# Kernel optimization log

Measured on AMD Instinct MI355X. Metric: run time of the kernel, lower is better.

Reference implementation:

```python
import jax, jax.numpy as jnp
import numpy as np

B, S, D, H = 4, 1024, 1024, 16
DH = D // H  # 64, per-head dim; FFN hidden = 2048
DFF = 2048

def setup_inputs() -> dict:
    key = jax.random.key(0)
    ks = jax.random.split(key, 6)
    x = jax.random.normal(ks[0], (B, S, D), dtype=jnp.float32)
    # Per-head q/k/v projection weights, stacked over heads: [H, D, DH].
    # Equivalent math to n_heads separate SelfAttentionLayer(d_head) calls + concat.
    sc_in = 1.0 / np.sqrt(D)
    Wq = jax.random.normal(ks[1], (H, D, DH), dtype=jnp.float32) * sc_in
    Wk = jax.random.normal(ks[2], (H, D, DH), dtype=jnp.float32) * sc_in
    Wv = jax.random.normal(ks[3], (H, D, DH), dtype=jnp.float32) * sc_in
    W1 = jax.random.normal(ks[4], (D, DFF), dtype=jnp.float32) * sc_in
    b1 = jnp.zeros((DFF,), dtype=jnp.float32)
    W2 = jax.random.normal(ks[5], (DFF, D), dtype=jnp.float32) * (1.0 / np.sqrt(DFF))
    b2 = jnp.zeros((D,), dtype=jnp.float32)
    return {"x": x, "Wq": Wq, "Wk": Wk, "Wv": Wv,
            "W1": W1, "b1": b1, "W2": W2, "b2": b2}

def reference(x, Wq, Wk, Wv, W1, b1, W2, b2):
    # Batched multi-head self-attention (math-equivalent to the per-head loop + concat).
    q = jnp.einsum('bsd,hde->bhse', x, Wq)          # [B,H,S,DH]
    k = jnp.einsum('bsd,hde->bhse', x, Wk)
    v = jnp.einsum('bsd,hde->bhse', x, Wv)
    scale = 1.0 / jnp.sqrt(jnp.asarray(q.shape[-1], q.dtype))
    scores = jnp.einsum('bhqe,bhke->bhqk', q, k) * scale  # [B,H,S,S]
    attn = jax.nn.softmax(scores, axis=-1)
    o = jnp.einsum('bhqk,bhke->bhqe', attn, v)      # [B,H,S,DH]
    h1 = o.transpose(0, 2, 1, 3).reshape(x.shape[0], x.shape[1], -1)  # concat heads -> [B,S,D]
    # FCLayer(2048, d): Dense(2048, relu) -> Dense(d)
    y = jax.nn.relu(h1 @ W1 + b1) @ W2 + b2
    return y
```

## Files before the change

kernel.cpp:

```cpp
#include <hip/hip_runtime.h>
#include <hip/hip_bf16.h>


typedef unsigned short u16;
typedef __attribute__((ext_vector_type(8))) short bfrag8;
typedef __attribute__((ext_vector_type(4))) float f32x4;

constexpr int Bb = 4, Ss = 1024, Dd = 1024, Hh = 16, DFF = 2048;

__device__ __forceinline__ u16 f2bf(float f) {
  unsigned u = __float_as_uint(f);
  return (u16)((u + 0x7fffu + ((u >> 16) & 1u)) >> 16);
}

__device__ __forceinline__ int swz(int byte) {
  return byte ^ (((byte >> 7) & 7) << 4);
}

__device__ __forceinline__ void gload16(const void* g, void* l) {
  __builtin_amdgcn_global_load_lds(
      (const __attribute__((address_space(1))) unsigned int*)g,
      (__attribute__((address_space(3))) unsigned int*)l, 16, 0, 0);
}

__global__ __launch_bounds__(256) void cvt_bf16(const float* __restrict__ in,
                                                u16* __restrict__ out, int n4) {
  int i = blockIdx.x * 256 + threadIdx.x;
  if (i >= n4) return;
  float4 v = ((const float4*)in)[i];
  ushort4 o = make_ushort4(f2bf(v.x), f2bf(v.y), f2bf(v.z), f2bf(v.w));
  *(ushort4*)(out + (size_t)i * 4) = o;
}

__device__ __forceinline__ void transpose64(const float* __restrict__ in,
                                            u16* __restrict__ out,
                                            int R, int C, int r0, int c0) {
  __shared__ float tile[64][65];
  const int t = threadIdx.x, cl = t & 63, rq = t >> 6;
#pragma unroll
  for (int i = 0; i < 16; ++i) {
    int rl = rq * 16 + i;
    tile[rl][cl] = in[(size_t)(r0 + rl) * C + c0 + cl];
  }
  __syncthreads();
#pragma unroll
  for (int i = 0; i < 16; ++i) {
    int oc = rq * 16 + i;
    out[(size_t)(c0 + oc) * R + r0 + cl] = f2bf(tile[cl][oc]);
  }
}

__global__ __launch_bounds__(256) void transpose_cvt(const float* __restrict__ in,
                                                     u16* __restrict__ out,
                                                     int R, int C) {
  transpose64(in, out, R, C, blockIdx.x * 64, blockIdx.y * 64);
}

__global__ __launch_bounds__(256) void qkv_transpose_cvt(
    const float* __restrict__ Wq, const float* __restrict__ Wk,
    const float* __restrict__ Wv, u16* __restrict__ out) {
  const int z = blockIdx.y;
  const int which = z >> 4, h = z & 15;
  const float* in = (which == 0 ? Wq : which == 1 ? Wk : Wv) + (size_t)h * 1024 * 64;
  u16* o = out + (size_t)z * 64 * 1024;
  transpose64(in, o, 1024, 64, blockIdx.x * 64, 0);
}

template <int EPI>
__global__ __launch_bounds__(256) void mfma_gemm(
    const u16* __restrict__ A, const u16* __restrict__ Bt,
    const float* __restrict__ bias, void* __restrict__ Cout, int N, int K) {
  __shared__ alignas(16) u16 Asm[128 * 32];
  __shared__ alignas(16) u16 Bsm[128 * 32];
  const int tid = threadIdx.x;
  const int wid = tid >> 6, lane = tid & 63;
  const int m0 = blockIdx.y * 128, n0 = blockIdx.x * 128;
  const int wr = wid >> 1, wc = wid & 1;
  const int fr = lane & 15, krow = lane >> 4;

  const int srow = tid >> 2;
  const int sk = (tid & 3) * 8;
  const u16* ga0 = A + (size_t)(m0 + srow) * K + sk;
  const u16* ga1 = A + (size_t)(m0 + srow + 64) * K + sk;
  const u16* gb0 = Bt + (size_t)(n0 + srow) * K + sk;
  const u16* gb1 = Bt + (size_t)(n0 + srow + 64) * K + sk;
  char* lA0 = (char*)Asm + tid * 16;
  char* lA1 = lA0 + 4096;
  char* lB0 = (char*)Bsm + tid * 16;
  char* lB1 = lB0 + 4096;

  f32x4 acc[4][4];
#pragma unroll
  for (int i = 0; i < 4; ++i)
#pragma unroll
    for (int j = 0; j < 4; ++j) acc[i][j] = (f32x4){0.f, 0.f, 0.f, 0.f};

  const char* pa = (const char*)Asm + (wr * 64 + fr) * 64 + krow * 16;
  const char* pb = (const char*)Bsm + (wc * 64 + fr) * 64 + krow * 16;

  for (int kt = 0; kt < K / 32; ++kt) {
    __syncthreads();
    gload16(ga0 + kt * 32, lA0);
    gload16(ga1 + kt * 32, lA1);
    gload16(gb0 + kt * 32, lB0);
    gload16(gb1 + kt * 32, lB1);
    __syncthreads();

    bfrag8 af[4], bfv[4];
#pragma unroll
    for (int i = 0; i < 4; ++i) af[i] = *(const bfrag8*)(pa + i * 1024);
#pragma unroll
    for (int j = 0; j < 4; ++j) bfv[j] = *(const bfrag8*)(pb + j * 1024);
#pragma unroll
    for (int i = 0; i < 4; ++i)
#pragma unroll
      for (int j = 0; j < 4; ++j)
        acc[i][j] = __builtin_amdgcn_mfma_f32_16x16x32_bf16(af[i], bfv[j], acc[i][j], 0, 0, 0);
  }

  const int orow = (lane >> 4) * 4;
  const int ocol = lane & 15;
#pragma unroll
  for (int i = 0; i < 4; ++i) {
#pragma unroll
    for (int j = 0; j < 4; ++j) {
      const int gn = n0 + wc * 64 + j * 16 + ocol;
      const int gm0 = m0 + wr * 64 + i * 16 + orow;
      if (EPI == 0) {
        const int which = gn >> 10, hh = (gn >> 6) & 15, e = gn & 63;
        const int bb = gm0 >> 10, s0 = gm0 & 1023;
        const int hb = hh * 4 + bb;
        u16* oq = (u16*)Cout;
        if (which < 2) {
#pragma unroll
          for (int r = 0; r < 4; ++r)
            oq[(size_t)which * 4194304 + ((size_t)hb * 1024 + s0 + r) * 64 + e] =
                f2bf(acc[i][j][r]);
        } else {
          ushort4 pk = make_ushort4(f2bf(acc[i][j][0]), f2bf(acc[i][j][1]),
                                    f2bf(acc[i][j][2]), f2bf(acc[i][j][3]));
          *(ushort4*)&oq[8388608 + ((size_t)hb * 64 + e) * 1024 + s0] = pk;
        }
      } else if (EPI == 1) {
#pragma unroll
        for (int r = 0; r < 4; ++r) {
          float v = fmaxf(acc[i][j][r] + bias[gn], 0.f);
          ((u16*)Cout)[(size_t)(gm0 + r) * N + gn] = f2bf(v);
        }
      } else {
#pragma unroll
        for (int r = 0; r < 4; ++r)
          ((float*)Cout)[(size_t)(gm0 + r) * N + gn] = acc[i][j][r] + bias[gn];
      }
    }
  }
}

__global__ __launch_bounds__(256) void attn_mfma(
    const u16* __restrict__ qb, const u16* __restrict__ kb,
    const u16* __restrict__ vtb, u16* __restrict__ h1) {
  __shared__ alignas(16) u16 Ks[64 * 64];
  __shared__ alignas(16) u16 Vs[64 * 64];
  __shared__ alignas(16) u16 Ps[4][32 * 64];
  const int tid = threadIdx.x, wid = tid >> 6, lane = tid & 63;
  const int hb = blockIdx.y, h = hb >> 2, b = hb & 3;
  const int q0 = blockIdx.x * 128 + wid * 32;
  const int fr = lane & 15, hi = lane >> 4;

  const u16* Qg = qb + ((size_t)hb * 1024 + q0) * 64;
  const u16* Kg = kb + (size_t)hb * 1024 * 64;
  const u16* Vg = vtb + (size_t)hb * 64 * 1024;
  char* Kw = (char*)Ks;
  char* Vw = (char*)Vs;
  char* Pw = (char*)Ps[wid];

  bfrag8 qf[2][2];
#pragma unroll
  for (int m = 0; m < 2; ++m)
#pragma unroll
    for (int kk = 0; kk < 2; ++kk)
      qf[m][kk] = *(const bfrag8*)(Qg + (m * 16 + fr) * 64 + kk * 32 + hi * 8);

  f32x4 acc_o[2][4];
#pragma unroll
  for (int m = 0; m < 2; ++m)
#pragma unroll
    for (int en = 0; en < 4; ++en) acc_o[m][en] = (f32x4){0.f, 0.f, 0.f, 0.f};
  float mrun[2][4], lrun[2][4];
#pragma unroll
  for (int m = 0; m < 2; ++m)
#pragma unroll
    for (int r = 0; r < 4; ++r) { mrun[m][r] = -3.0e38f; lrun[m][r] = 0.f; }

  const int srow0 = tid >> 3;
  const int scol = (tid & 7) * 8;

  for (int kt = 0; kt < 16; ++kt) {
    __syncthreads();
    bfrag8 kv0 = *(const bfrag8*)(Kg + (size_t)(kt * 64 + srow0) * 64 + scol);
    bfrag8 kv1 = *(const bfrag8*)(Kg + (size_t)(kt * 64 + srow0 + 32) * 64 + scol);
    bfrag8 vv0 = *(const bfrag8*)(Vg + (size_t)srow0 * 1024 + kt * 64 + scol);
    bfrag8 vv1 = *(const bfrag8*)(Vg + (size_t)(srow0 + 32) * 1024 + kt * 64 + scol);
    *(bfrag8*)(Kw + swz(srow0 * 128 + scol * 2)) = kv0;
    *(bfrag8*)(Kw + swz((srow0 + 32) * 128 + scol * 2)) = kv1;
    *(bfrag8*)(Vw + swz(srow0 * 128 + scol * 2)) = vv0;
    *(bfrag8*)(Vw + swz((srow0 + 32) * 128 + scol * 2)) = vv1;
    __syncthreads();

    f32x4 sc[2][4];
#pragma unroll
    for (int m = 0; m < 2; ++m)
#pragma unroll
      for (int kn = 0; kn < 4; ++kn) sc[m][kn] = (f32x4){0.f, 0.f, 0.f, 0.f};
    bfrag8 kf[4][2];
#pragma unroll
    for (int kn = 0; kn < 4; ++kn)
#pragma unroll
      for (int kk = 0; kk < 2; ++kk)
        kf[kn][kk] = *(const bfrag8*)(Kw + swz((kn * 16 + fr) * 128 + kk * 64 + hi * 16));
#pragma unroll
    for (int m = 0; m < 2; ++m)
#pragma unroll
      for (int kn = 0; kn < 4; ++kn)
#pragma unroll
        for (int kk = 0; kk < 2; ++kk)
          sc[m][kn] = __builtin_amdgcn_mfma_f32_16x16x32_bf16(qf[m][kk], kf[kn][kk],
                                                              sc[m][kn], 0, 0, 0);

#pragma unroll
    for (int m = 0; m < 2; ++m) {
      float ss[4][4];
#pragma unroll
      for (int kn = 0; kn < 4; ++kn)
#pragma unroll
        for (int r = 0; r < 4; ++r) ss[kn][r] = sc[m][kn][r] * 0.125f;
      float rmax[4];
#pragma unroll
      for (int r = 0; r < 4; ++r)
        rmax[r] = fmaxf(fmaxf(ss[0][r], ss[1][r]), fmaxf(ss[2][r], ss[3][r]));
#pragma unroll
      for (int mk = 1; mk <= 8; mk <<= 1)
#pragma unroll
        for (int r = 0; r < 4; ++r)
          rmax[r] = fmaxf(rmax[r], __shfl_xor(rmax[r], mk));
      float scl[4];
#pragma unroll
      for (int r = 0; r < 4; ++r) {
        const float mnew = fmaxf(mrun[m][r], rmax[r]);
        scl[r] = __expf(mrun[m][r] - mnew);
        mrun[m][r] = mnew;
      }
#pragma unroll
      for (int kn = 0; kn < 4; ++kn)
#pragma unroll
        for (int r = 0; r < 4; ++r) ss[kn][r] = __expf(ss[kn][r] - mrun[m][r]);
      float ps[4];
#pragma unroll
      for (int r = 0; r < 4; ++r)
        ps[r] = (ss[0][r] + ss[1][r]) + (ss[2][r] + ss[3][r]);
#pragma unroll
      for (int mk = 1; mk <= 8; mk <<= 1)
#pragma unroll
        for (int r = 0; r < 4; ++r) ps[r] += __shfl_xor(ps[r], mk);
#pragma unroll
      for (int r = 0; r < 4; ++r) lrun[m][r] = lrun[m][r] * scl[r] + ps[r];
#pragma unroll
      for (int en = 0; en < 4; ++en)
#pragma unroll
        for (int r = 0; r < 4; ++r) acc_o[m][en][r] *= scl[r];
#pragma unroll
      for (int kn = 0; kn < 4; ++kn)
#pragma unroll
        for (int r = 0; r < 4; ++r)
          *(u16*)(Pw + swz((m * 16 + hi * 4 + r) * 128 + (kn * 16 + fr) * 2)) =
              f2bf(ss[kn][r]);
    }

    bfrag8 vf[4][2], pf[2][2];
#pragma unroll
    for (int en = 0; en < 4; ++en)
#pragma unroll
      for (int kf2 = 0; kf2 < 2; ++kf2)
        vf[en][kf2] = *(const bfrag8*)(Vw + swz((en * 16 + fr) * 128 + kf2 * 64 + hi * 16));
#pragma unroll
    for (int m = 0; m < 2; ++m)
#pragma unroll
      for (int kf2 = 0; kf2 < 2; ++kf2)
        pf[m][kf2] = *(const bfrag8*)(Pw + swz((m * 16 + fr) * 128 + kf2 * 64 + hi * 16));
#pragma unroll
    for (int m = 0; m < 2; ++m)
#pragma unroll
      for (int en = 0; en < 4; ++en)
#pragma unroll
        for (int kf2 = 0; kf2 < 2; ++kf2)
          acc_o[m][en] = __builtin_amdgcn_mfma_f32_16x16x32_bf16(pf[m][kf2], vf[en][kf2],
                                                                 acc_o[m][en], 0, 0, 0);
  }

#pragma unroll
  for (int m = 0; m < 2; ++m) {
    float inv[4];
#pragma unroll
    for (int r = 0; r < 4; ++r) inv[r] = 1.f / lrun[m][r];
#pragma unroll
    for (int en = 0; en < 4; ++en)
#pragma unroll
      for (int r = 0; r < 4; ++r) {
        const int s = q0 + m * 16 + hi * 4 + r;
        h1[((size_t)(b * 1024 + s)) * 1024 + h * 64 + en * 16 + fr] =
            f2bf(acc_o[m][en][r] * inv[r]);
      }
  }
}

extern "C" void kernel_launch(void* const* d_in, const int* in_sizes, int n_in,
                              void* d_out, int out_size, void* d_ws, size_t ws_size,
                              hipStream_t stream) {
  const float* x  = (const float*)d_in[0];
  const float* Wq = (const float*)d_in[1];
  const float* Wk = (const float*)d_in[2];
  const float* Wv = (const float*)d_in[3];
  const float* W1 = (const float*)d_in[4];
  const float* b1 = (const float*)d_in[5];
  const float* W2 = (const float*)d_in[6];
  const float* b2 = (const float*)d_in[7];

  const size_t MB = 1u << 20;
  char* w = (char*)d_ws;
  u16* qkvb  = (u16*)w;
  u16* Xb    = (u16*)(w + 24 * MB);
  u16* Wqkvt = (u16*)(w + 32 * MB);
  u16* W1t   = (u16*)(w + 38 * MB);
  u16* W2t   = (u16*)(w + 42 * MB);
  u16* h1b   = (u16*)(w + 46 * MB);
  u16* ffb   = (u16*)(w + 54 * MB);

  cvt_bf16<<<4096, 256, 0, stream>>>(x, Xb, 1048576);
  qkv_transpose_cvt<<<dim3(16, 48), 256, 0, stream>>>(Wq, Wk, Wv, Wqkvt);
  transpose_cvt<<<dim3(16, 32), 256, 0, stream>>>(W1, W1t, 1024, 2048);
  transpose_cvt<<<dim3(32, 16), 256, 0, stream>>>(W2, W2t, 2048, 1024);

  mfma_gemm<0><<<dim3(24, 32), 256, 0, stream>>>(Xb, Wqkvt, nullptr, qkvb, 3072, 1024);
  attn_mfma<<<dim3(8, 64), 256, 0, stream>>>(qkvb, qkvb + 4194304, qkvb + 8388608, h1b);
  mfma_gemm<1><<<dim3(16, 32), 256, 0, stream>>>(h1b, W1t, b1, ffb, 2048, 1024);
  mfma_gemm<2><<<dim3(8, 32), 256, 0, stream>>>(ffb, W2t, b2, d_out, 1024, 2048);
}
```

Measured before the change: 277.6 us.

## Rewrite attention to register-resident exp2 softmax, add XCD block swizzle and N64 GEMM

```diff
diff --git a/kernel.cpp b/kernel.cpp
--- a/kernel.cpp
+++ b/kernel.cpp
@@ -5,22 +5,26 @@
 typedef unsigned short u16;
 typedef __attribute__((ext_vector_type(8))) short bfrag8;
 typedef __attribute__((ext_vector_type(4))) float f32x4;
+typedef __attribute__((ext_vector_type(4))) int ix4;
 
 constexpr int Bb = 4, Ss = 1024, Dd = 1024, Hh = 16, DFF = 2048;
+constexpr float QSCALE = 0.18033688011112042f;
 
 __device__ __forceinline__ u16 f2bf(float f) {
   unsigned u = __float_as_uint(f);
   return (u16)((u + 0x7fffu + ((u >> 16) & 1u)) >> 16);
-}
-
-__device__ __forceinline__ int swz(int byte) {
-  return byte ^ (((byte >> 7) & 7) << 4);
 }
 
 __device__ __forceinline__ void gload16(const void* g, void* l) {
   __builtin_amdgcn_global_load_lds(
       (const __attribute__((address_space(1))) unsigned int*)g,
       (__attribute__((address_space(3))) unsigned int*)l, 16, 0, 0);
+}
+
+__device__ __forceinline__ int xcd_swz() {
+  const int id = blockIdx.y * gridDim.x + blockIdx.x;
+  const int cpx = (gridDim.x * gridDim.y) >> 3;
+  return (id & 7) * cpx + (id >> 3);
 }
 
 __global__ __launch_bounds__(256) void cvt_bf16(const float* __restrict__ in,
@@ -74,7 +78,8 @@
   __shared__ alignas(16) u16 Bsm[128 * 32];
   const int tid = threadIdx.x;
   const int wid = tid >> 6, lane = tid & 63;
-  const int m0 = blockIdx.y * 128, n0 = blockIdx.x * 128;
+  const int nid = xcd_swz();
+  const int m0 = (nid / gridDim.x) * 128, n0 = (nid % gridDim.x) * 128;
   const int wr = wid >> 1, wc = wid & 1;
   const int fr = lane & 15, krow = lane >> 4;
 
@@ -131,11 +136,14 @@
         const int bb = gm0 >> 10, s0 = gm0 & 1023;
         const int hb = hh * 4 + bb;
         u16* oq = (u16*)Cout;
-        if (which < 2) {
+        if (which == 0) {
 #pragma unroll
           for (int r = 0; r < 4; ++r)
-            oq[(size_t)which * 4194304 + ((size_t)hb * 1024 + s0 + r) * 64 + e] =
-                f2bf(acc[i][j][r]);
+            oq[((size_t)hb * 1024 + s0 + r) * 64 + e] = f2bf(acc[i][j][r] * QSCALE);
+        } else if (which == 1) {
+#pragma unroll
+          for (int r = 0; r < 4; ++r)
+            oq[4194304 + ((size_t)hb * 1024 + s0 + r) * 64 + e] = f2bf(acc[i][j][r]);
         } else {
           ushort4 pk = make_ushort4(f2bf(acc[i][j][0]), f2bf(acc[i][j][1]),
                                     f2bf(acc[i][j][2]), f2bf(acc[i][j][3]));
@@ -156,23 +164,81 @@
   }
 }
 
-__global__ __launch_bounds__(256) void attn_mfma(
+__global__ __launch_bounds__(256) void mfma_gemm_n64(
+    const u16* __restrict__ A, const u16* __restrict__ Bt,
+    const float* __restrict__ bias, float* __restrict__ Cout, int N, int K) {
+  __shared__ alignas(16) u16 Asm[128 * 32];
+  __shared__ alignas(16) u16 Bsm[64 * 32];
+  const int tid = threadIdx.x;
+  const int wid = tid >> 6, lane = tid & 63;
+  const int nid = xcd_swz();
+  const int m0 = (nid / gridDim.x) * 128, n0 = (nid % gridDim.x) * 64;
+  const int fr = lane & 15, krow = lane >> 4;
+
+  const int srow = tid >> 2;
+  const int sk = (tid & 3) * 8;
+  const u16* ga0 = A + (size_t)(m0 + srow) * K + sk;
+  const u16* ga1 = A + (size_t)(m0 + srow + 64) * K + sk;
+  const u16* gb0 = Bt + (size_t)(n0 + srow) * K + sk;
+  char* lA0 = (char*)Asm + tid * 16;
+  char* lA1 = lA0 + 4096;
+  char* lB0 = (char*)Bsm + tid * 16;
+
+  f32x4 acc[2][4];
+#pragma unroll
+  for (int i = 0; i < 2; ++i)
+#pragma unroll
+    for (int j = 0; j < 4; ++j) acc[i][j] = (f32x4){0.f, 0.f, 0.f, 0.f};
+
+  const char* pa = (const char*)Asm + (wid * 32 + fr) * 64 + krow * 16;
+  const char* pb = (const char*)Bsm + fr * 64 + krow * 16;
+
+  for (int kt = 0; kt < K / 32; ++kt) {
+    __syncthreads();
+    gload16(ga0 + kt * 32, lA0);
+    gload16(ga1 + kt * 32, lA1);
+    gload16(gb0 + kt * 32, lB0);
+    __syncthreads();
+
+    bfrag8 af[2], bfv[4];
+#pragma unroll
+    for (int i = 0; i < 2; ++i) af[i] = *(const bfrag8*)(pa + i * 1024);
+#pragma unroll
+    for (int j = 0; j < 4; ++j) bfv[j] = *(const bfrag8*)(pb + j * 1024);
+#pragma unroll
+    for (int i = 0; i < 2; ++i)
+#pragma unroll
+      for (int j = 0; j < 4; ++j)
+        acc[i][j] = __builtin_amdgcn_mfma_f32_16x16x32_bf16(af[i], bfv[j], acc[i][j], 0, 0, 0);
+  }
+
+  const int orow = (lane >> 4) * 4;
+  const int ocol = lane & 15;
+#pragma unroll
+  for (int i = 0; i < 2; ++i)
+#pragma unroll
+    for (int j = 0; j < 4; ++j) {
+      const int gn = n0 + j * 16 + ocol;
+      const int gm0 = m0 + wid * 32 + i * 16 + orow;
+#pragma unroll
+      for (int r = 0; r < 4; ++r)
+        Cout[(size_t)(gm0 + r) * N + gn] = acc[i][j][r] + bias[gn];
+    }
+}
+
+__global__ __launch_bounds__(256, 2) void attn_mfma(
     const u16* __restrict__ qb, const u16* __restrict__ kb,
     const u16* __restrict__ vtb, u16* __restrict__ h1) {
-  __shared__ alignas(16) u16 Ks[64 * 64];
-  __shared__ alignas(16) u16 Vs[64 * 64];
-  __shared__ alignas(16) u16 Ps[4][32 * 64];
   const int tid = threadIdx.x, wid = tid >> 6, lane = tid & 63;
-  const int hb = blockIdx.y, h = hb >> 2, b = hb & 3;
-  const int q0 = blockIdx.x * 128 + wid * 32;
+  const int nid = xcd_swz();
+  const int qx = nid & 7, hb = nid >> 3;
+  const int h = hb >> 2, b = hb & 3;
+  const int q0 = qx * 128 + wid * 32;
   const int fr = lane & 15, hi = lane >> 4;
 
   const u16* Qg = qb + ((size_t)hb * 1024 + q0) * 64;
   const u16* Kg = kb + (size_t)hb * 1024 * 64;
   const u16* Vg = vtb + (size_t)hb * 64 * 1024;
-  char* Kw = (char*)Ks;
-  char* Vw = (char*)Vs;
-  char* Pw = (char*)Ps[wid];
 
   bfrag8 qf[2][2];
 #pragma unroll
@@ -181,136 +247,121 @@
     for (int kk = 0; kk < 2; ++kk)
       qf[m][kk] = *(const bfrag8*)(Qg + (m * 16 + fr) * 64 + kk * 32 + hi * 8);
 
-  f32x4 acc_o[2][4];
+  f32x4 acc2[2][4];
 #pragma unroll
   for (int m = 0; m < 2; ++m)
 #pragma unroll
-    for (int en = 0; en < 4; ++en) acc_o[m][en] = (f32x4){0.f, 0.f, 0.f, 0.f};
-  float mrun[2][4], lrun[2][4];
-#pragma unroll
-  for (int m = 0; m < 2; ++m)
-#pragma unroll
-    for (int r = 0; r < 4; ++r) { mrun[m][r] = -3.0e38f; lrun[m][r] = 0.f; }
-
-  const int srow0 = tid >> 3;
-  const int scol = (tid & 7) * 8;
-
-  for (int kt = 0; kt < 16; ++kt) {
-    __syncthreads();
-    bfrag8 kv0 = *(const bfrag8*)(Kg + (size_t)(kt * 64 + srow0) * 64 + scol);
-    bfrag8 kv1 = *(const bfrag8*)(Kg + (size_t)(kt * 64 + srow0 + 32) * 64 + scol);
-    bfrag8 vv0 = *(const bfrag8*)(Vg + (size_t)srow0 * 1024 + kt * 64 + scol);
-    bfrag8 vv1 = *(const bfrag8*)(Vg + (size_t)(srow0 + 32) * 1024 + kt * 64 + scol);
-    *(bfrag8*)(Kw + swz(srow0 * 128 + scol * 2)) = kv0;
-    *(bfrag8*)(Kw + swz((srow0 + 32) * 128 + scol * 2)) = kv1;
-    *(bfrag8*)(Vw + swz(srow0 * 128 + scol * 2)) = vv0;
-    *(bfrag8*)(Vw + swz((srow0 + 32) * 128 + scol * 2)) = vv1;
-    __syncthreads();
-
-    f32x4 sc[2][4];
-#pragma unroll
-    for (int m = 0; m < 2; ++m)
-#pragma unroll
-      for (int kn = 0; kn < 4; ++kn) sc[m][kn] = (f32x4){0.f, 0.f, 0.f, 0.f};
-    bfrag8 kf[4][2];
-#pragma unroll
-    for (int kn = 0; kn < 4; ++kn)
-#pragma unroll
-      for (int kk = 0; kk < 2; ++kk)
-        kf[kn][kk] = *(const bfrag8*)(Kw + swz((kn * 16 + fr) * 128 + kk * 64 + hi * 16));
-#pragma unroll
-    for (int m = 0; m < 2; ++m)
-#pragma unroll
-      for (int kn = 0; kn < 4; ++kn)
-#pragma unroll
-        for (int kk = 0; kk < 2; ++kk)
-          sc[m][kn] = __builtin_amdgcn_mfma_f32_16x16x32_bf16(qf[m][kk], kf[kn][kk],
-                                                              sc[m][kn], 0, 0, 0);
-
-#pragma unroll
-    for (int m = 0; m < 2; ++m) {
-      float ss[4][4];
-#pragma unroll
-      for (int kn = 0; kn < 4; ++kn)
-#pragma unroll
-        for (int r = 0; r < 4; ++r) ss[kn][r] = sc[m][kn][r] * 0.125f;
-      float rmax[4];
-#pragma unroll
-      for (int r = 0; r < 4; ++r)
-        rmax[r] = fmaxf(fmaxf(ss[0][r], ss[1][r]), fmaxf(ss[2][r], ss[3][r]));
-#pragma unroll
-      for (int mk = 1; mk <= 8; mk <<= 1)
-#pragma unroll
-        for (int r = 0; r < 4; ++r)
-          rmax[r] = fmaxf(rmax[r], __shfl_xor(rmax[r], mk));
-      float scl[4];
-#pragma unroll
-      for (int r = 0; r < 4; ++r) {
-        const float mnew = fmaxf(mrun[m][r], rmax[r]);
-        scl[r] = __expf(mrun[m][r] - mnew);
-        mrun[m][r] = mnew;
-      }
-#pragma unroll
-      for (int kn = 0; kn < 4; ++kn)
-#pragma unroll
-        for (int r = 0; r < 4; ++r) ss[kn][r] = __expf(ss[kn][r] - mrun[m][r]);
-      float ps[4];
-#pragma unroll
-      for (int r = 0; r < 4; ++r)
-        ps[r] = (ss[0][r] + ss[1][r]) + (ss[2][r] + ss[3][r]);
-#pragma unroll
-      for (int mk = 1; mk <= 8; mk <<= 1)
-#pragma unroll
-        for (int r = 0; r < 4; ++r) ps[r] += __shfl_xor(ps[r], mk);
-#pragma unroll
-      for (int r = 0; r < 4; ++r) lrun[m][r] = lrun[m][r] * scl[r] + ps[r];
-#pragma unroll
-      for (int en = 0; en < 4; ++en)
-#pragma unroll
-        for (int r = 0; r < 4; ++r) acc_o[m][en][r] *= scl[r];
-#pragma unroll
-      for (int kn = 0; kn < 4; ++kn)
-#pragma unroll
-        for (int r = 0; r < 4; ++r)
-          *(u16*)(Pw + swz((m * 16 + hi * 4 + r) * 128 + (kn * 16 + fr) * 2)) =
-              f2bf(ss[kn][r]);
+    for (int en = 0; en < 4; ++en) acc2[m][en] = (f32x4){0.f, 0.f, 0.f, 0.f};
+  float mrun[2] = {-1e30f, -1e30f}, lrun[2] = {0.f, 0.f};
+
+  const int addrA = ((lane & 15) + ((lane & 16) << 1)) << 2;
+  const int addrB = addrA + 64;
+  const bool hiSel = (lane >= 32);
+
+  bfrag8 kfA[4][2], vfA[4][2], kfB[4][2], vfB[4][2];
+
+#define LOAD_KV(kf, vf, kt)                                                    \
+  {                                                                            \
+    _Pragma("unroll") for (int kn = 0; kn < 4; ++kn)                           \
+        _Pragma("unroll") for (int kk = 0; kk < 2; ++kk) {                     \
+      kf[kn][kk] = *(const bfrag8*)(Kg + (size_t)((kt)*64 + kn * 16 + fr) * 64 \
+                                    + kk * 32 + hi * 8);                       \
+      vf[kn][kk] = *(const bfrag8*)(Vg + (size_t)(kn * 16 + fr) * 1024         \
+                                    + (kt)*64 + kk * 32 + hi * 8);             \
+    }                                                                          \
+  }
+
+#define TILE_STEP(kf, vf)                                                      \
+  {                                                                            \
+    f32x4 sc2[2][4];                                                           \
+    __builtin_amdgcn_s_setprio(1);                                             \
+    _Pragma("unroll") for (int m = 0; m < 2; ++m)                              \
+        _Pragma("unroll") for (int kn = 0; kn < 4; ++kn) {                     \
+      f32x4 t = (f32x4){0.f, 0.f, 0.f, 0.f};                                   \
+      t = __builtin_amdgcn_mfma_f32_16x16x32_bf16(kf[kn][0], qf[m][0], t, 0, 0, 0); \
+      t = __builtin_amdgcn_mfma_f32_16x16x32_bf16(kf[kn][1], qf[m][1], t, 0, 0, 0); \
+      sc2[m][kn] = t;                                                          \
+    }                                                                          \
+    __builtin_amdgcn_s_setprio(0);                                             \
+    int pk[2][4][2];                                                           \
+    _Pragma("unroll") for (int m = 0; m < 2; ++m) {                            \
+      float cm = -1e30f;                                                       \
+      _Pragma("unroll") for (int kn = 0; kn < 4; ++kn)                         \
+          _Pragma("unroll") for (int r = 0; r < 4; ++r)                        \
+              cm = fmaxf(cm, sc2[m][kn][r]);                                   \
+      cm = fmaxf(cm, __shfl_xor(cm, 16));                                      \
+      cm = fmaxf(cm, __shfl_xor(cm, 32));                                      \
+      const float mnew = fmaxf(mrun[m], cm);                                   \
+      const float scl = exp2f(mrun[m] - mnew);                                 \
+      mrun[m] = mnew;                                                          \
+      float psum = 0.f;                                                        \
+      float p[4][4];                                                           \
+      _Pragma("unroll") for (int kn = 0; kn < 4; ++kn)                         \
+          _Pragma("unroll") for (int r = 0; r < 4; ++r) {                      \
+        p[kn][r] = exp2f(sc2[m][kn][r] - mnew);                                \
+        psum += p[kn][r];                                                      \
+      }                                                                        \
+      psum += __shfl_xor(psum, 16);                                            \
+      psum += __shfl_xor(psum, 32);                                            \
+      lrun[m] = lrun[m] * scl + psum;                                          \
+      _Pragma("unroll") for (int en = 0; en < 4; ++en)                         \
+          acc2[m][en] = acc2[m][en] * scl;                                     \
+      _Pragma("unroll") for (int kn = 0; kn < 4; ++kn) {                       \
+        asm("v_cvt_pk_bf16_f32 %0, %1, %2"                                     \
+            : "=v"(pk[m][kn][0]) : "v"(p[kn][0]), "v"(p[kn][1]));              \
+        asm("v_cvt_pk_bf16_f32 %0, %1, %2"                                     \
+            : "=v"(pk[m][kn][1]) : "v"(p[kn][2]), "v"(p[kn][3]));              \
+      }                                                                        \
+    }                                                                          \
+    bfrag8 pfrag[2][2];                                                        \
+    _Pragma("unroll") for (int m = 0; m < 2; ++m)                              \
+        _Pragma("unroll") for (int kk = 0; kk < 2; ++kk) {                     \
+      int w[4];                                                                \
+      _Pragma("unroll") for (int wi = 0; wi < 2; ++wi) {                       \
+        int t0 = __builtin_amdgcn_ds_bpermute(addrA, pk[m][2 * kk][wi]);       \
+        int t1 = __builtin_amdgcn_ds_bpermute(addrA, pk[m][2 * kk + 1][wi]);   \
+        w[wi] = hiSel ? t1 : t0;                                               \
+        t0 = __builtin_amdgcn_ds_bpermute(addrB, pk[m][2 * kk][wi]);           \
+        t1 = __builtin_amdgcn_ds_bpermute(addrB, pk[m][2 * kk + 1][wi]);       \
+        w[2 + wi] = hiSel ? t1 : t0;                                           \
+      }                                                                        \
+      ix4 tmp = (ix4){w[0], w[1], w[2], w[3]};                                 \
+      pfrag[m][kk] = __builtin_bit_cast(bfrag8, tmp);                          \
+    }                                                                          \
+    __builtin_amdgcn_s_setprio(1);                                             \
+    _Pragma("unroll") for (int m = 0; m < 2; ++m)                              \
+        _Pragma("unroll") for (int en = 0; en < 4; ++en) {                     \
+      acc2[m][en] = __builtin_amdgcn_mfma_f32_16x16x32_bf16(                   \
+          vf[en][0], pfrag[m][0], acc2[m][en], 0, 0, 0);                       \
+      acc2[m][en] = __builtin_amdgcn_mfma_f32_16x16x32_bf16(                   \
+          vf[en][1], pfrag[m][1], acc2[m][en], 0, 0, 0);                       \
+    }                                                                          \
+    __builtin_amdgcn_s_setprio(0);                                             \
+  }
+
+  LOAD_KV(kfA, vfA, 0);
+  for (int kt = 0; kt < 16; kt += 2) {
+    if (kt + 1 < 16) LOAD_KV(kfB, vfB, kt + 1);
+    TILE_STEP(kfA, vfA);
+    if (kt + 2 < 16) LOAD_KV(kfA, vfA, kt + 2);
+    TILE_STEP(kfB, vfB);
+  }
+
+#pragma unroll
+  for (int m = 0; m < 2; ++m) {
+    const float inv = 1.f / lrun[m];
+    const int s = q0 + m * 16 + fr;
+    u16* op = h1 + ((size_t)(b * 1024 + s)) * 1024 + h * 64 + hi * 4;
+#pragma unroll
+    for (int en = 0; en < 4; ++en) {
+      ushort4 o = make_ushort4(
+          f2bf(acc2[m][en][0] * inv), f2bf(acc2[m][en][1] * inv),
+          f2bf(acc2[m][en][2] * inv), f2bf(acc2[m][en][3] * inv));
+      *(ushort4*)(op + en * 16) = o;
     }
-
-    bfrag8 vf[4][2], pf[2][2];
-#pragma unroll
-    for (int en = 0; en < 4; ++en)
-#pragma unroll
-      for (int kf2 = 0; kf2 < 2; ++kf2)
-        vf[en][kf2] = *(const bfrag8*)(Vw + swz((en * 16 + fr) * 128 + kf2 * 64 + hi * 16));
-#pragma unroll
-    for (int m = 0; m < 2; ++m)
-#pragma unroll
-      for (int kf2 = 0; kf2 < 2; ++kf2)
-        pf[m][kf2] = *(const bfrag8*)(Pw + swz((m * 16 + fr) * 128 + kf2 * 64 + hi * 16));
-#pragma unroll
-    for (int m = 0; m < 2; ++m)
-#pragma unroll
-      for (int en = 0; en < 4; ++en)
-#pragma unroll
-        for (int kf2 = 0; kf2 < 2; ++kf2)
-          acc_o[m][en] = __builtin_amdgcn_mfma_f32_16x16x32_bf16(pf[m][kf2], vf[en][kf2],
-                                                                 acc_o[m][en], 0, 0, 0);
-  }
-
-#pragma unroll
-  for (int m = 0; m < 2; ++m) {
-    float inv[4];
-#pragma unroll
-    for (int r = 0; r < 4; ++r) inv[r] = 1.f / lrun[m][r];
-#pragma unroll
-    for (int en = 0; en < 4; ++en)
-#pragma unroll
-      for (int r = 0; r < 4; ++r) {
-        const int s = q0 + m * 16 + hi * 4 + r;
-        h1[((size_t)(b * 1024 + s)) * 1024 + h * 64 + en * 16 + fr] =
-            f2bf(acc_o[m][en][r] * inv[r]);
-      }
-  }
+  }
+#undef LOAD_KV
+#undef TILE_STEP
 }
 
 extern "C" void kernel_launch(void* const* d_in, const int* in_sizes, int n_in,
@@ -343,5 +394,5 @@
   mfma_gemm<0><<<dim3(24, 32), 256, 0, stream>>>(Xb, Wqkvt, nullptr, qkvb, 3072, 1024);
   attn_mfma<<<dim3(8, 64), 256, 0, stream>>>(qkvb, qkvb + 4194304, qkvb + 8388608, h1b);
   mfma_gemm<1><<<dim3(16, 32), 256, 0, stream>>>(h1b, W1t, b1, ffb, 2048, 1024);
-  mfma_gemm<2><<<dim3(8, 32), 256, 0, stream>>>(ffb, W2t, b2, d_out, 1024, 2048);
-}
+  mfma_gemm_n64<<<dim3(16, 32), 256, 0, stream>>>(ffb, W2t, b2, (float*)d_out, 1024, 2048);
+}
```

Result: no change. 279.1 us (+0.5%).
